# Optimization experiments

Hardware: AMD Instinct MI355X
Metric: run time of the kernel (lower is better)

The kernel has to match this reference:

```python
import jax, jax.numpy as jnp
import numpy as np

N = 50000      # nodes
DEG = 12       # in-degree per node
E = N * DEG    # 600000 edges
IN_FEATS = 256
H_FEATS = 128
NUM_LAYERS = 2
BN_EPS = 1e-5
PD_EPS = 1e-6  # torch pairwise_distance eps


def _batch_norm(x):
    # BatchNorm1d(affine=False) in training mode: per-feature batch stats, biased var
    m = x.mean(axis=0)
    v = ((x - m) ** 2).mean(axis=0)
    return (x - m) / jnp.sqrt(v + BN_EPS)


def setup_inputs() -> dict:
    key = jax.random.key(0)
    ks = jax.random.split(key, 6)
    x = jax.random.normal(ks[0], (N, IN_FEATS), dtype=jnp.float32)
    # xavier-uniform-like scales
    s_init = float(np.sqrt(6.0 / (IN_FEATS + H_FEATS)))
    s_h = float(np.sqrt(6.0 / (2 * H_FEATS)))
    W_init = jax.random.uniform(ks[1], (IN_FEATS, H_FEATS), jnp.float32, -s_init, s_init)
    W0 = jax.random.uniform(ks[2], (H_FEATS, H_FEATS), jnp.float32, -s_h, s_h)
    W1 = jax.random.uniform(ks[3], (H_FEATS, H_FEATS), jnp.float32, -s_h, s_h)
    b0 = jnp.zeros((H_FEATS,), jnp.float32)
    b1 = jnp.zeros((H_FEATS,), jnp.float32)
    src = jax.random.randint(ks[4], (E,), 0, N, dtype=jnp.int32)
    dst = jnp.repeat(jnp.arange(N, dtype=jnp.int32), DEG)  # every node has in-degree DEG
    return {"x": x, "W_init": W_init, "W0": W0, "b0": b0, "W1": W1, "b1": b1,
            "src": src, "dst": dst}


def _embed_nodes(x, W_init, Ws, bs, src, dst):
    # h = act(norm(x @ init_weight)); then GraphConv(norm='none') layers
    h = jax.nn.relu(_batch_norm(x @ W_init))
    for W, b in zip(Ws, bs):
        msg = h[src] @ W                       # [E, H]
        agg = jax.ops.segment_sum(msg, dst, num_segments=N)  # sum aggregation
        h = jax.nn.relu(_batch_norm(agg + b))
    return h


def _nonparametric_embedding(x, src, dst, deg):
    # GIN(apply_func=None, eps=-1, aggregator='mean') == mean of in-neighbors
    h = jax.nn.relu(_batch_norm(x))
    for _ in range(NUM_LAYERS):
        agg = jax.ops.segment_sum(h[src], dst, num_segments=N) / deg[:, None]
        h = jax.nn.relu(_batch_norm(agg))
    return h


def _mean_edge_dist(h, src, dst, deg):
    # apply_edges: pairwise_distance(src, dst); pull: scatter-mean onto dst
    d = jnp.linalg.norm(h[src] - h[dst] + PD_EPS, axis=1)  # [E]
    return jax.ops.segment_sum(d, dst, num_segments=N) / deg  # [N]


def reference(x, W_init, W0, b0, W1, b1, src, dst):
    deg = jnp.maximum(
        jax.ops.segment_sum(jnp.ones((E,), jnp.float32), dst, num_segments=N), 1.0)
    h_final = _embed_nodes(x, W_init, (W0, W1), (b0, b1), src, dst)
    # nonparametric target distances (detached in original)
    h_nonpar = _nonparametric_embedding(jax.lax.stop_gradient(x), src, dst, deg)
    d_nonpar = jax.lax.stop_gradient(_mean_edge_dist(h_nonpar, src, dst, deg))
    d_par = _mean_edge_dist(h_final, src, dst, deg)
    loss = jnp.mean((jnp.log(d_par) - jnp.log(d_nonpar)) ** 2)
    return (h_final, loss)
```

## Files before the change

### kernel.cpp

```cpp
#include <hip/hip_runtime.h>
#include <hip/hip_fp16.h>
#include <math.h>

#define DEG 12
#define BN_EPS 1e-5f
#define PD_EPS 1e-6f

using uint = unsigned int;

typedef _Float16 fp16x8 __attribute__((ext_vector_type(8)));
typedef float f32x2 __attribute__((ext_vector_type(2)));
typedef float f32x4 __attribute__((ext_vector_type(4)));

__device__ inline float2 h2f2(uint u) {
  __half2 h; __builtin_memcpy(&h, &u, 4);
  return __half22float2(h);
}
__device__ inline uint f2h2(float a, float b) {
  __half2 h = __floats2half2_rn(a, b);
  uint u; __builtin_memcpy(&u, &h, 4);
  return u;
}
__device__ inline f32x2 q2f_lo(uint u) { return __builtin_amdgcn_cvt_pk_f32_fp8(u, false); }
__device__ inline f32x2 q2f_hi(uint u) { return __builtin_amdgcn_cvt_pk_f32_fp8(u, true); }
__device__ inline uint f4_to_q(float a, float b, float c, float d) {
  uint w = 0;
  w = __builtin_amdgcn_cvt_pk_fp8_f32(a, b, w, false);
  w = __builtin_amdgcn_cvt_pk_fp8_f32(c, d, w, true);
  return w;
}

#define STATS_NB 256

template<int F>
__global__ __launch_bounds__(512) void stats_h_part(const __half* __restrict__ in,
                                                    float* __restrict__ parts, int M) {
  const int G = F / 8;
  __shared__ float redA[512 * 8];
  __shared__ float redB[512 * 8];
  int tid = threadIdx.x;
  int total = M * G;
  float s[8] = {0,0,0,0,0,0,0,0}, q[8] = {0,0,0,0,0,0,0,0};
  for (int i = blockIdx.x * 512 + tid; i < total; i += gridDim.x * 512) {
    uint4 raw = ((const uint4*)in)[i];
    float2 v0 = h2f2(raw.x), v1 = h2f2(raw.y), v2 = h2f2(raw.z), v3 = h2f2(raw.w);
    float v[8] = {v0.x, v0.y, v1.x, v1.y, v2.x, v2.y, v3.x, v3.y};
#pragma unroll
    for (int j = 0; j < 8; ++j) { s[j] += v[j]; q[j] += v[j] * v[j]; }
  }
#pragma unroll
  for (int j = 0; j < 8; ++j) { redA[tid * 8 + j] = s[j]; redB[tid * 8 + j] = q[j]; }
  __syncthreads();
  if (tid < F) {
    int c = tid >> 3, j = tid & 7;
    float as = 0.f, aq = 0.f;
#pragma unroll 4
    for (int r = 0; r < 512 / G; ++r) {
      as += redA[(r * G + c) * 8 + j];
      aq += redB[(r * G + c) * 8 + j];
    }
    parts[blockIdx.x * 2 * F + tid]     = as;
    parts[blockIdx.x * 2 * F + F + tid] = aq;
  }
}

template<int F>
__global__ __launch_bounds__(512) void stats_q_part(const uint* __restrict__ in,
                                                    float* __restrict__ parts, int M) {
  const int G = F / 8;
  __shared__ float redA[512 * 8];
  __shared__ float redB[512 * 8];
  int tid = threadIdx.x;
  int total = M * G;
  float s[8] = {0,0,0,0,0,0,0,0}, q[8] = {0,0,0,0,0,0,0,0};
  for (int i = blockIdx.x * 512 + tid; i < total; i += gridDim.x * 512) {
    uint2 raw = ((const uint2*)in)[i];
    f32x2 a = q2f_lo(raw.x), b = q2f_hi(raw.x), c = q2f_lo(raw.y), d = q2f_hi(raw.y);
    float v[8] = {a.x, a.y, b.x, b.y, c.x, c.y, d.x, d.y};
#pragma unroll
    for (int j = 0; j < 8; ++j) { s[j] += v[j]; q[j] += v[j] * v[j]; }
  }
#pragma unroll
  for (int j = 0; j < 8; ++j) { redA[tid * 8 + j] = s[j]; redB[tid * 8 + j] = q[j]; }
  __syncthreads();
  if (tid < F) {
    int c = tid >> 3, j = tid & 7;
    float as = 0.f, aq = 0.f;
#pragma unroll 4
    for (int r = 0; r < 512 / G; ++r) {
      as += redA[(r * G + c) * 8 + j];
      aq += redB[(r * G + c) * 8 + j];
    }
    parts[blockIdx.x * 2 * F + tid]     = as;
    parts[blockIdx.x * 2 * F + F + tid] = aq;
  }
}

template<int F>
__global__ __launch_bounds__(512) void stats_f_part(const float* __restrict__ in,
                                                    float* __restrict__ parts, int M) {
  const int G = F / 4;
  __shared__ float redA[512 * 4];
  __shared__ float redB[512 * 4];
  int tid = threadIdx.x;
  int total = M * G;
  float s[4] = {0,0,0,0}, q[4] = {0,0,0,0};
  for (int i = blockIdx.x * 512 + tid; i < total; i += gridDim.x * 512) {
    float4 v = ((const float4*)in)[i];
    float w[4] = {v.x, v.y, v.z, v.w};
#pragma unroll
    for (int j = 0; j < 4; ++j) { s[j] += w[j]; q[j] += w[j] * w[j]; }
  }
#pragma unroll
  for (int j = 0; j < 4; ++j) { redA[tid * 4 + j] = s[j]; redB[tid * 4 + j] = q[j]; }
  __syncthreads();
  if (tid < F) {
    int c = tid >> 2, j = tid & 3;
    float as = 0.f, aq = 0.f;
#pragma unroll 4
    for (int r = 0; r < 512 / G; ++r) {
      as += redA[(r * G + c) * 4 + j];
      aq += redB[(r * G + c) * 4 + j];
    }
    parts[blockIdx.x * 2 * F + tid]     = as;
    parts[blockIdx.x * 2 * F + F + tid] = aq;
  }
}

template<int F>
__global__ __launch_bounds__(1024) void stats_final(const float* __restrict__ parts,
                                                    int M, float* __restrict__ stats) {
  const int OUT = 2 * F;
  const int T   = 1024 / OUT;
  __shared__ float red[1024];
  int tid = threadIdx.x;
  int o = tid & (OUT - 1);
  int c = tid / OUT;
  float s = 0.f;
#pragma unroll 16
  for (int b = c; b < STATS_NB; b += T) s += parts[b * OUT + o];
  red[tid] = s;
  __syncthreads();
  if (tid < OUT) {
    float acc = red[tid];
#pragma unroll
    for (int cc = 1; cc < T; ++cc) acc += red[cc * OUT + tid];
    red[tid] = acc;
  }
  __syncthreads();
  if (tid < F) {
    float mean = red[tid] / (float)M;
    float var  = red[F + tid] / (float)M - mean * mean;
    stats[tid]     = mean;
    stats[F + tid] = 1.0f / sqrtf(var + BN_EPS);
  }
}

__global__ void transpose_cast(const float* __restrict__ W, __half* __restrict__ WT, int K) {
  int idx = blockIdx.x * 256 + threadIdx.x;
  if (idx >= 128 * K) return;
  int n = idx / K, k = idx - n * K;
  WT[idx] = __float2half(W[(size_t)k * 128 + n]);
}

__global__ __launch_bounds__(256) void gemm_x(
    const float* __restrict__ A, const float* __restrict__ stats,
    const __half* __restrict__ WT, __half* __restrict__ C,
    uint* __restrict__ xq, int M) {
  __shared__ uint4 Bs4[64 * 32];
  char* Bs = (char*)Bs4;
  int tid = threadIdx.x;
  int wave = tid >> 6, lane = tid & 63;
  int row0 = blockIdx.x * 64 + wave * 16;
  int r = lane & 15, kg = lane >> 4;
  int arow = row0 + r; if (arow >= M) arow = M - 1;
  bool vrow = (row0 + r) < M;
  const float* Ap = A + (size_t)arow * 256 + kg * 8;

  fp16x8 af[8];
#pragma unroll
  for (int a = 0; a < 8; ++a) {
    int c0 = kg * 8 + a * 32;
    float4 lo = *(const float4*)(Ap + a * 32);
    float4 hi = *(const float4*)(Ap + a * 32 + 4);
    af[a][0] = (_Float16)lo.x; af[a][1] = (_Float16)lo.y;
    af[a][2] = (_Float16)lo.z; af[a][3] = (_Float16)lo.w;
    af[a][4] = (_Float16)hi.x; af[a][5] = (_Float16)hi.y;
    af[a][6] = (_Float16)hi.z; af[a][7] = (_Float16)hi.w;
    float4 m0 = *(const float4*)(stats + c0);
    float4 m1 = *(const float4*)(stats + c0 + 4);
    float4 v0 = *(const float4*)(stats + 256 + c0);
    float4 v1 = *(const float4*)(stats + 256 + c0 + 4);
    float w0 = fmaxf((lo.x - m0.x) * v0.x, 0.f);
    float w1 = fmaxf((lo.y - m0.y) * v0.y, 0.f);
    float w2 = fmaxf((lo.z - m0.z) * v0.z, 0.f);
    float w3 = fmaxf((lo.w - m0.w) * v0.w, 0.f);
    float w4 = fmaxf((hi.x - m1.x) * v1.x, 0.f);
    float w5 = fmaxf((hi.y - m1.y) * v1.y, 0.f);
    float w6 = fmaxf((hi.z - m1.z) * v1.z, 0.f);
    float w7 = fmaxf((hi.w - m1.w) * v1.w, 0.f);
    if (vrow) {
      uint2 q; q.x = f4_to_q(w0, w1, w2, w3); q.y = f4_to_q(w4, w5, w6, w7);
      ((uint2*)xq)[(size_t)arow * 32 + (c0 >> 3)] = q;
    }
  }

  f32x4 acc[8];
#pragma unroll
  for (int n = 0; n < 8; ++n) acc[n] = (f32x4){0.f, 0.f, 0.f, 0.f};
  const uint4* Wg = (const uint4*)WT;

#pragma unroll
  for (int ph = 0; ph < 2; ++ph) {
    __syncthreads();
#pragma unroll
    for (int i = 0; i < 8; ++i) {
      int idx = tid + i * 256;
      int rw = idx >> 5, c16 = idx & 31;
      *(uint4*)(Bs + rw * 512 + ((c16 * 16) ^ ((rw & 7) << 4))) = Wg[ph * 2048 + idx];
    }
    __syncthreads();
#pragma unroll
    for (int a = 0; a < 8; ++a) {
#pragma unroll
      for (int n4 = 0; n4 < 4; ++n4) {
        int rw = n4 * 16 + r;
        fp16x8 bf = *(const fp16x8*)(Bs + rw * 512 + ((kg * 16 + a * 64) ^ ((r & 7) << 4)));
        acc[ph * 4 + n4] = __builtin_amdgcn_mfma_f32_16x16x32_f16(af[a], bf, acc[ph * 4 + n4], 0, 0, 0);
      }
    }
  }
#pragma unroll
  for (int n = 0; n < 8; ++n) {
    int col = n * 16 + r;
#pragma unroll
    for (int rr = 0; rr < 4; ++rr) {
      int row = row0 + kg * 4 + rr;
      if (row < M) C[(size_t)row * 128 + col] = __float2half(acc[n][rr]);
    }
  }
}

template<bool OUT_HALF>
__global__ __launch_bounds__(256) void gemm_128(
    const __half* __restrict__ A, const __half* __restrict__ WT,
    const float* __restrict__ bias, void* __restrict__ Cv, int M) {
  __shared__ uint4 Bs4[128 * 16];
  char* Bs = (char*)Bs4;
  int tid = threadIdx.x;
  const uint4* Wg = (const uint4*)WT;
#pragma unroll
  for (int i = 0; i < 8; ++i) {
    int idx = tid + i * 256;
    int rw = idx >> 4, c16 = idx & 15;
    *(uint4*)(Bs + rw * 256 + ((c16 * 16) ^ ((rw & 7) << 4))) = Wg[idx];
  }
  int wave = tid >> 6, lane = tid & 63;
  int row0 = blockIdx.x * 64 + wave * 16;
  int r = lane & 15, kg = lane >> 4;
  int arow = row0 + r; if (arow >= M) arow = M - 1;
  const _Float16* Ap = (const _Float16*)A + (size_t)arow * 128 + kg * 8;

  fp16x8 af[4];
#pragma unroll
  for (int a = 0; a < 4; ++a) af[a] = *(const fp16x8*)(Ap + a * 32);

  __syncthreads();
  f32x4 acc[8];
#pragma unroll
  for (int n = 0; n < 8; ++n) acc[n] = (f32x4){0.f, 0.f, 0.f, 0.f};
#pragma unroll
  for (int a = 0; a < 4; ++a) {
#pragma unroll
    for (int n = 0; n < 8; ++n) {
      int rw = n * 16 + r;
      fp16x8 bf = *(const fp16x8*)(Bs + rw * 256 + ((kg * 16 + a * 64) ^ ((r & 7) << 4)));
      acc[n] = __builtin_amdgcn_mfma_f32_16x16x32_f16(af[a], bf, acc[n], 0, 0, 0);
    }
  }
#pragma unroll
  for (int n = 0; n < 8; ++n) {
    int col = n * 16 + r;
    float bv = bias[col];
#pragma unroll
    for (int rr = 0; rr < 4; ++rr) {
      int row = row0 + kg * 4 + rr;
      if (row >= M) continue;
      float v = acc[n][rr] + bv;
      if (OUT_HALF) ((__half*)Cv)[(size_t)row * 128 + col] = __float2half(v);
      else          ((float*)Cv)[(size_t)row * 128 + col] = v;
    }
  }
}

template<int F, bool BNRELU>
__global__ __launch_bounds__(256) void agg_n(
    const __half* __restrict__ H, const float* __restrict__ stats,
    const int* __restrict__ src, __half* __restrict__ outh,
    float scale, int n_nodes) {
  const int LPN = F / 8;
  const int NPB = 256 / LPN;
  int tid  = threadIdx.x;
  int g    = tid / LPN;
  int lig  = tid % LPN;
  int node = blockIdx.x * NPB + g;
  if (node >= n_nodes) return;
  float m[8], iv[8];
  if (BNRELU) {
#pragma unroll
    for (int j = 0; j < 8; ++j) {
      m[j]  = stats[lig * 8 + j];
      iv[j] = stats[F + lig * 8 + j];
    }
  }
  int lane = tid & 63;
  int grpStart = lane & (63 ^ (LPN - 1));
  int se = 0;
  if ((lane & (LPN - 1)) < DEG) se = src[node * DEG + (lane & (LPN - 1))];

  const uint4* HH = (const uint4*)H;
  float a[8] = {0,0,0,0,0,0,0,0};
#pragma unroll
  for (int e = 0; e < DEG; ++e) {
    int s = __shfl(se, grpStart + e);
    uint4 raw = HH[(size_t)s * LPN + lig];
    float2 v0 = h2f2(raw.x), v1 = h2f2(raw.y), v2 = h2f2(raw.z), v3 = h2f2(raw.w);
    float w[8] = {v0.x, v0.y, v1.x, v1.y, v2.x, v2.y, v3.x, v3.y};
    if (BNRELU) {
#pragma unroll
      for (int j = 0; j < 8; ++j) w[j] = fmaxf((w[j] - m[j]) * iv[j], 0.f);
    }
#pragma unroll
    for (int j = 0; j < 8; ++j) a[j] += w[j];
  }
  uint4 w;
  w.x = f2h2(a[0] * scale, a[1] * scale);
  w.y = f2h2(a[2] * scale, a[3] * scale);
  w.z = f2h2(a[4] * scale, a[5] * scale);
  w.w = f2h2(a[6] * scale, a[7] * scale);
  ((uint4*)outh)[(size_t)node * LPN + lig] = w;
}

template<int F, bool BNRELU>
__global__ __launch_bounds__(256) void agg_q(
    const uint* __restrict__ H, const float* __restrict__ stats,
    const int* __restrict__ src, uint* __restrict__ outq,
    float scale, int n_nodes) {
  const int LPN = F / 8;
  const int NPB = 256 / LPN;
  int tid  = threadIdx.x;
  int g    = tid / LPN;
  int lig  = tid % LPN;
  int node = blockIdx.x * NPB + g;
  if (node >= n_nodes) return;
  float m[8], iv[8];
  if (BNRELU) {
#pragma unroll
    for (int j = 0; j < 8; ++j) {
      m[j]  = stats[lig * 8 + j];
      iv[j] = stats[F + lig * 8 + j];
    }
  }
  int lane = tid & 63;
  int grpStart = lane & (63 ^ (LPN - 1));
  int se = 0;
  if ((lane & (LPN - 1)) < DEG) se = src[node * DEG + (lane & (LPN - 1))];

  const uint2* HH = (const uint2*)H;
  float a[8] = {0,0,0,0,0,0,0,0};
#pragma unroll
  for (int e = 0; e < DEG; ++e) {
    int s = __shfl(se, grpStart + e);
    uint2 raw = HH[(size_t)s * LPN + lig];
    f32x2 p0 = q2f_lo(raw.x), p1 = q2f_hi(raw.x), p2 = q2f_lo(raw.y), p3 = q2f_hi(raw.y);
    float w[8] = {p0.x, p0.y, p1.x, p1.y, p2.x, p2.y, p3.x, p3.y};
    if (BNRELU) {
#pragma unroll
      for (int j = 0; j < 8; ++j) w[j] = fmaxf((w[j] - m[j]) * iv[j], 0.f);
    }
#pragma unroll
    for (int j = 0; j < 8; ++j) a[j] += w[j];
  }
  uint2 w;
  w.x = f4_to_q(a[0] * scale, a[1] * scale, a[2] * scale, a[3] * scale);
  w.y = f4_to_q(a[4] * scale, a[5] * scale, a[6] * scale, a[7] * scale);
  ((uint2*)outq)[(size_t)node * LPN + lig] = w;
}

template<int F>
__global__ __launch_bounds__(256) void dist_q(
    const uint* __restrict__ H, const int* __restrict__ src,
    float* __restrict__ out, int n_nodes) {
  const int LPN = 16;
  const int NPB = 256 / LPN;
  const int NU2 = F / 128;
  int tid  = threadIdx.x;
  int g    = tid / LPN;
  int lig  = tid % LPN;
  int node = blockIdx.x * NPB + g;
  if (node >= n_nodes) return;
  int lane = tid & 63;
  int grpStart = lane & 48;
  int se = 0;
  if ((lane & 15) < DEG) se = src[node * DEG + (lane & 15)];

  const uint2* HH = (const uint2*)H;
  float oe[NU2 * 8];
#pragma unroll
  for (int k = 0; k < NU2; ++k) {
    uint2 o = HH[(size_t)node * (F / 8) + lig * NU2 + k];
    f32x2 p0 = q2f_lo(o.x), p1 = q2f_hi(o.x), p2 = q2f_lo(o.y), p3 = q2f_hi(o.y);
    oe[k*8+0] = PD_EPS - p0.x; oe[k*8+1] = PD_EPS - p0.y;
    oe[k*8+2] = PD_EPS - p1.x; oe[k*8+3] = PD_EPS - p1.y;
    oe[k*8+4] = PD_EPS - p2.x; oe[k*8+5] = PD_EPS - p2.y;
    oe[k*8+6] = PD_EPS - p3.x; oe[k*8+7] = PD_EPS - p3.y;
  }

  float dsum = 0.f;
#pragma unroll
  for (int e = 0; e < DEG; ++e) {
    int s = __shfl(se, grpStart + e);
    float sq = 0.f;
#pragma unroll
    for (int k = 0; k < NU2; ++k) {
      uint2 raw = HH[(size_t)s * (F / 8) + lig * NU2 + k];
      f32x2 p0 = q2f_lo(raw.x), p1 = q2f_hi(raw.x), p2 = q2f_lo(raw.y), p3 = q2f_hi(raw.y);
      float w[8] = {p0.x, p0.y, p1.x, p1.y, p2.x, p2.y, p3.x, p3.y};
#pragma unroll
      for (int j = 0; j < 8; ++j) {
        float d = w[j] + oe[k*8+j];
        sq = fmaf(d, d, sq);
      }
    }
#pragma unroll
    for (int mask = 1; mask < LPN; mask <<= 1) sq += __shfl_xor(sq, mask);
    dsum += sqrtf(sq);
  }
  if (lig == 0) out[node] = dsum * (1.0f / (float)DEG);
}

template<int F>
__global__ void bnrelu_q2q(const uint* __restrict__ in, const float* __restrict__ stats,
                           uint* __restrict__ out, int total1) {
  for (int idx = blockIdx.x * blockDim.x + threadIdx.x; idx < total1;
       idx += gridDim.x * blockDim.x) {
    uint raw = in[idx];
    int f0 = (idx & (F / 4 - 1)) * 4;
    f32x2 p0 = q2f_lo(raw), p1 = q2f_hi(raw);
    float w0 = fmaxf((p0.x - stats[f0+0]) * stats[F+f0+0], 0.f);
    float w1 = fmaxf((p0.y - stats[f0+1]) * stats[F+f0+1], 0.f);
    float w2 = fmaxf((p1.x - stats[f0+2]) * stats[F+f0+2], 0.f);
    float w3 = fmaxf((p1.y - stats[f0+3]) * stats[F+f0+3], 0.f);
    out[idx] = f4_to_q(w0, w1, w2, w3);
  }
}

template<int F>
__global__ void bnrelu_dual(const float* __restrict__ in, const float* __restrict__ stats,
                            float* __restrict__ outf, uint* __restrict__ outq, int total4) {
  for (int idx = blockIdx.x * blockDim.x + threadIdx.x; idx < total4;
       idx += gridDim.x * blockDim.x) {
    float4 v = ((const float4*)in)[idx];
    int f0 = (idx & (F / 4 - 1)) * 4;
    float w0 = fmaxf((v.x - stats[f0+0]) * stats[F+f0+0], 0.f);
    float w1 = fmaxf((v.y - stats[f0+1]) * stats[F+f0+1], 0.f);
    float w2 = fmaxf((v.z - stats[f0+2]) * stats[F+f0+2], 0.f);
    float w3 = fmaxf((v.w - stats[f0+3]) * stats[F+f0+3], 0.f);
    ((float4*)outf)[idx] = make_float4(w0, w1, w2, w3);
    outq[idx] = f4_to_q(w0, w1, w2, w3);
  }
}

__global__ void loss_partial(const float* __restrict__ dpar, const float* __restrict__ dnp,
                             float* __restrict__ parts, int n) {
  __shared__ float red[256];
  float acc = 0.f;
  for (int i = blockIdx.x * 256 + threadIdx.x; i < n; i += gridDim.x * 256) {
    float t = logf(dpar[i]) - logf(dnp[i]);
    acc += t * t;
  }
  red[threadIdx.x] = acc;
  __syncthreads();
  for (int s = 128; s; s >>= 1) {
    if (threadIdx.x < s) red[threadIdx.x] += red[threadIdx.x + s];
    __syncthreads();
  }
  if (threadIdx.x == 0) parts[blockIdx.x] = red[0];
}

__global__ void loss_final(const float* __restrict__ parts, int nb,
                           float* __restrict__ out, float inv_n) {
  if (threadIdx.x == 0) {
    float s = 0.f;
    for (int i = 0; i < nb; ++i) s += parts[i];
    *out = s * inv_n;
  }
}

extern "C" void kernel_launch(void* const* d_in, const int* in_sizes, int n_in,
                              void* d_out, int out_size, void* d_ws, size_t ws_size,
                              hipStream_t stream) {
  const float* x  = (const float*)d_in[0];
  const float* Wi = (const float*)d_in[1];
  const float* W0 = (const float*)d_in[2];
  const float* b0 = (const float*)d_in[3];
  const float* W1 = (const float*)d_in[4];
  const float* b1 = (const float*)d_in[5];
  const int*  src = (const int*)d_in[6];

  const int N = in_sizes[0] / 256;
  float* out = (float*)d_out;

  const size_t NF = (size_t)N * 128;
  float* S1 = (float*)d_ws;
  float* S2 = S1 + NF;
  float* S3 = S2 + NF;
  float* aux = S3 + NF;
  float* dpar   = aux;
  float* dnp    = dpar + N;
  float* parts  = dnp + N;
  float* s_x    = parts + STATS_NB * 512;
  float* s_y0   = s_x + 512;
  float* s_z1   = s_y0 + 256;
  float* s_z2   = s_z1 + 256;
  float* s_a1   = s_z2 + 256;
  float* s_a2   = s_a1 + 512;
  float* lparts = s_a2 + 512;
  __half* WiT   = (__half*)(lparts + 64);
  __half* W0T   = (__half*)(lparts + 64 + 16384);
  __half* W1T   = (__half*)(lparts + 64 + 24576);
  uint*   xq    = (uint*)(lparts + 64 + 32768);

  __half* y0h = (__half*)S1;
  __half* H0h = (__half*)S2;
  __half* z1h = (__half*)S1;
  __half* H1h = (__half*)S2;
  float*  z2  = S3;
  uint* hq   = (uint*)S1;
  uint* A1q  = (uint*)S3;
  uint* A2q  = (uint*)S2;
  uint* A2nq = (uint*)S1;

  const int g64   = (N + 63) / 64;
  const int g128a = N / 16;
  const int gaggq = N / 8;
  const int gdist = N / 16;

  transpose_cast<<<(128 * 256 + 255) / 256, 256, 0, stream>>>(Wi, WiT, 256);
  transpose_cast<<<(128 * 128 + 255) / 256, 256, 0, stream>>>(W0, W0T, 128);
  transpose_cast<<<(128 * 128 + 255) / 256, 256, 0, stream>>>(W1, W1T, 128);

  stats_f_part<256><<<STATS_NB, 512, 0, stream>>>(x, parts, N);
  stats_final<256><<<1, 1024, 0, stream>>>(parts, N, s_x);

  gemm_x<<<g64, 256, 0, stream>>>(x, s_x, WiT, y0h, xq, N);
  stats_h_part<128><<<STATS_NB, 512, 0, stream>>>(y0h, parts, N);
  stats_final<128><<<1, 1024, 0, stream>>>(parts, N, s_y0);
  agg_n<128, true><<<g128a, 256, 0, stream>>>(y0h, s_y0, src, H0h, 1.0f, N);
  gemm_128<true><<<g64, 256, 0, stream>>>(H0h, W0T, b0, z1h, N);
  stats_h_part<128><<<STATS_NB, 512, 0, stream>>>(z1h, parts, N);
  stats_final<128><<<1, 1024, 0, stream>>>(parts, N, s_z1);
  agg_n<128, true><<<g128a, 256, 0, stream>>>(z1h, s_z1, src, H1h, 1.0f, N);
  gemm_128<false><<<g64, 256, 0, stream>>>(H1h, W1T, b1, z2, N);
  stats_f_part<128><<<STATS_NB, 512, 0, stream>>>(z2, parts, N);
  stats_final<128><<<1, 1024, 0, stream>>>(parts, N, s_z2);
  bnrelu_dual<128><<<2048, 256, 0, stream>>>(z2, s_z2, out, hq, N * 32);
  dist_q<128><<<gdist, 256, 0, stream>>>(hq, src, dpar, N);

  agg_q<256, false><<<gaggq, 256, 0, stream>>>(xq, nullptr, src, A1q, 1.0f / DEG, N);
  stats_q_part<256><<<STATS_NB, 512, 0, stream>>>(A1q, parts, N);
  stats_final<256><<<1, 1024, 0, stream>>>(parts, N, s_a1);
  agg_q<256, true><<<gaggq, 256, 0, stream>>>(A1q, s_a1, src, A2q, 1.0f / DEG, N);
  stats_q_part<256><<<STATS_NB, 512, 0, stream>>>(A2q, parts, N);
  stats_final<256><<<1, 1024, 0, stream>>>(parts, N, s_a2);
  bnrelu_q2q<256><<<2048, 256, 0, stream>>>(A2q, s_a2, A2nq, N * 64);
  dist_q<256><<<gdist, 256, 0, stream>>>(A2nq, src, dnp, N);

  loss_partial<<<64, 256, 0, stream>>>(dpar, dnp, lparts, N);
  loss_final<<<1, 64, 0, stream>>>(lparts, 64, out + (size_t)N * 128, 1.0f / (float)N);
}
```

Measured before the change: 277.2 us.

## Fuse column statistics into GEMM epilogues and store last GEMM output in half

Each GEMM now reduces per-column sums and sums of squares of its fp32 accumulators into per-block partials. A final reduction over g64 blocks replaces the separate stats pass that re-read the fp16 output. The last GEMM writes fp16 instead of fp32, and the BN/ReLU pass reads it with 8-wide loads. The three weight transposes are merged into one launch. This removes three stats kernels and part of the memory traffic, but adds shared-memory reductions and syncs to every GEMM block, gives stats_final about 780 partials to sum instead of 256, and rounds z2 to fp16 before normalization.

```diff
diff --git a/kernel.cpp b/kernel.cpp
--- a/kernel.cpp
+++ b/kernel.cpp
@@ -31,38 +31,6 @@
 }
 
 #define STATS_NB 256
-
-template<int F>
-__global__ __launch_bounds__(512) void stats_h_part(const __half* __restrict__ in,
-                                                    float* __restrict__ parts, int M) {
-  const int G = F / 8;
-  __shared__ float redA[512 * 8];
-  __shared__ float redB[512 * 8];
-  int tid = threadIdx.x;
-  int total = M * G;
-  float s[8] = {0,0,0,0,0,0,0,0}, q[8] = {0,0,0,0,0,0,0,0};
-  for (int i = blockIdx.x * 512 + tid; i < total; i += gridDim.x * 512) {
-    uint4 raw = ((const uint4*)in)[i];
-    float2 v0 = h2f2(raw.x), v1 = h2f2(raw.y), v2 = h2f2(raw.z), v3 = h2f2(raw.w);
-    float v[8] = {v0.x, v0.y, v1.x, v1.y, v2.x, v2.y, v3.x, v3.y};
-#pragma unroll
-    for (int j = 0; j < 8; ++j) { s[j] += v[j]; q[j] += v[j] * v[j]; }
-  }
-#pragma unroll
-  for (int j = 0; j < 8; ++j) { redA[tid * 8 + j] = s[j]; redB[tid * 8 + j] = q[j]; }
-  __syncthreads();
-  if (tid < F) {
-    int c = tid >> 3, j = tid & 7;
-    float as = 0.f, aq = 0.f;
-#pragma unroll 4
-    for (int r = 0; r < 512 / G; ++r) {
-      as += redA[(r * G + c) * 8 + j];
-      aq += redB[(r * G + c) * 8 + j];
-    }
-    parts[blockIdx.x * 2 * F + tid]     = as;
-    parts[blockIdx.x * 2 * F + F + tid] = aq;
-  }
-}
 
 template<int F>
 __global__ __launch_bounds__(512) void stats_q_part(const uint* __restrict__ in,
@@ -129,7 +97,7 @@
 
 template<int F>
 __global__ __launch_bounds__(1024) void stats_final(const float* __restrict__ parts,
-                                                    int M, float* __restrict__ stats) {
+                                                    int nb, int M, float* __restrict__ stats) {
   const int OUT = 2 * F;
   const int T   = 1024 / OUT;
   __shared__ float red[1024];
@@ -138,7 +106,7 @@
   int c = tid / OUT;
   float s = 0.f;
 #pragma unroll 16
-  for (int b = c; b < STATS_NB; b += T) s += parts[b * OUT + o];
+  for (int b = c; b < nb; b += T) s += parts[(size_t)b * OUT + o];
   red[tid] = s;
   __syncthreads();
   if (tid < OUT) {
@@ -156,17 +124,67 @@
   }
 }
 
-__global__ void transpose_cast(const float* __restrict__ W, __half* __restrict__ WT, int K) {
+__global__ void transpose_all(const float* __restrict__ Wi, const float* __restrict__ W0,
+                              const float* __restrict__ W1, __half* __restrict__ WiT,
+                              __half* __restrict__ W0T, __half* __restrict__ W1T) {
   int idx = blockIdx.x * 256 + threadIdx.x;
-  if (idx >= 128 * K) return;
-  int n = idx / K, k = idx - n * K;
-  WT[idx] = __float2half(W[(size_t)k * 128 + n]);
+  if (idx < 32768) {
+    int n = idx / 256, k = idx - n * 256;
+    WiT[idx] = __float2half(Wi[(size_t)k * 128 + n]);
+  } else if (idx < 49152) {
+    int i = idx - 32768; int n = i / 128, k = i - n * 128;
+    W0T[i] = __float2half(W0[(size_t)k * 128 + n]);
+  } else if (idx < 65536) {
+    int i = idx - 49152; int n = i / 128, k = i - n * 128;
+    W1T[i] = __float2half(W1[(size_t)k * 128 + n]);
+  }
+}
+
+__device__ __forceinline__ void colstats_epilogue_128(
+    void* scratch, const f32x4* acc, int row0w, int M,
+    float* __restrict__ parts, int bid, int tid, int kg, int r) {
+  float* red = (float*)scratch;
+  int slot = (tid >> 6) * 4 + kg;
+  __syncthreads();
+#pragma unroll
+  for (int n = 0; n < 8; ++n) {
+    float s = 0.f;
+#pragma unroll
+    for (int rr = 0; rr < 4; ++rr)
+      if (row0w + kg * 4 + rr < M) s += acc[n][rr];
+    red[slot * 128 + n * 16 + r] = s;
+  }
+  __syncthreads();
+  if (tid < 128) {
+    float s = 0.f;
+#pragma unroll
+    for (int i = 0; i < 16; ++i) s += red[i * 128 + tid];
+    parts[(size_t)bid * 256 + tid] = s;
+  }
+  __syncthreads();
+#pragma unroll
+  for (int n = 0; n < 8; ++n) {
+    float q = 0.f;
+#pragma unroll
+    for (int rr = 0; rr < 4; ++rr) {
+      float v = (row0w + kg * 4 + rr < M) ? acc[n][rr] : 0.f;
+      q += v * v;
+    }
+    red[slot * 128 + n * 16 + r] = q;
+  }
+  __syncthreads();
+  if (tid < 128) {
+    float q = 0.f;
+#pragma unroll
+    for (int i = 0; i < 16; ++i) q += red[i * 128 + tid];
+    parts[(size_t)bid * 256 + 128 + tid] = q;
+  }
 }
 
 __global__ __launch_bounds__(256) void gemm_x(
     const float* __restrict__ A, const float* __restrict__ stats,
     const __half* __restrict__ WT, __half* __restrict__ C,
-    uint* __restrict__ xq, int M) {
+    uint* __restrict__ xq, float* __restrict__ parts, int M) {
   __shared__ uint4 Bs4[64 * 32];
   char* Bs = (char*)Bs4;
   int tid = threadIdx.x;
@@ -239,12 +257,13 @@
       if (row < M) C[(size_t)row * 128 + col] = __float2half(acc[n][rr]);
     }
   }
-}
-
-template<bool OUT_HALF>
+  colstats_epilogue_128(Bs, acc, row0, M, parts, blockIdx.x, tid, kg, r);
+}
+
 __global__ __launch_bounds__(256) void gemm_128(
     const __half* __restrict__ A, const __half* __restrict__ WT,
-    const float* __restrict__ bias, void* __restrict__ Cv, int M) {
+    const float* __restrict__ bias, __half* __restrict__ C,
+    float* __restrict__ parts, int M) {
   __shared__ uint4 Bs4[128 * 16];
   char* Bs = (char*)Bs4;
   int tid = threadIdx.x;
@@ -284,13 +303,12 @@
     float bv = bias[col];
 #pragma unroll
     for (int rr = 0; rr < 4; ++rr) {
+      acc[n][rr] += bv;
       int row = row0 + kg * 4 + rr;
-      if (row >= M) continue;
-      float v = acc[n][rr] + bv;
-      if (OUT_HALF) ((__half*)Cv)[(size_t)row * 128 + col] = __float2half(v);
-      else          ((float*)Cv)[(size_t)row * 128 + col] = v;
-    }
-  }
+      if (row < M) C[(size_t)row * 128 + col] = __float2half(acc[n][rr]);
+    }
+  }
+  colstats_epilogue_128(Bs, acc, row0, M, parts, blockIdx.x, tid, kg, r);
 }
 
 template<int F, bool BNRELU>
@@ -456,18 +474,25 @@
 }
 
 template<int F>
-__global__ void bnrelu_dual(const float* __restrict__ in, const float* __restrict__ stats,
-                            float* __restrict__ outf, uint* __restrict__ outq, int total4) {
-  for (int idx = blockIdx.x * blockDim.x + threadIdx.x; idx < total4;
+__global__ void bnrelu_dual_h(const __half* __restrict__ in, const float* __restrict__ stats,
+                              float* __restrict__ outf, uint* __restrict__ outq, int total8) {
+  for (int idx = blockIdx.x * blockDim.x + threadIdx.x; idx < total8;
        idx += gridDim.x * blockDim.x) {
-    float4 v = ((const float4*)in)[idx];
-    int f0 = (idx & (F / 4 - 1)) * 4;
-    float w0 = fmaxf((v.x - stats[f0+0]) * stats[F+f0+0], 0.f);
-    float w1 = fmaxf((v.y - stats[f0+1]) * stats[F+f0+1], 0.f);
-    float w2 = fmaxf((v.z - stats[f0+2]) * stats[F+f0+2], 0.f);
-    float w3 = fmaxf((v.w - stats[f0+3]) * stats[F+f0+3], 0.f);
-    ((float4*)outf)[idx] = make_float4(w0, w1, w2, w3);
-    outq[idx] = f4_to_q(w0, w1, w2, w3);
+    uint4 raw = ((const uint4*)in)[idx];
+    int f0 = (idx & (F / 8 - 1)) * 8;
+    float2 v0 = h2f2(raw.x), v1 = h2f2(raw.y), v2 = h2f2(raw.z), v3 = h2f2(raw.w);
+    float w0 = fmaxf((v0.x - stats[f0+0]) * stats[F+f0+0], 0.f);
+    float w1 = fmaxf((v0.y - stats[f0+1]) * stats[F+f0+1], 0.f);
+    float w2 = fmaxf((v1.x - stats[f0+2]) * stats[F+f0+2], 0.f);
+    float w3 = fmaxf((v1.y - stats[f0+3]) * stats[F+f0+3], 0.f);
+    float w4 = fmaxf((v2.x - stats[f0+4]) * stats[F+f0+4], 0.f);
+    float w5 = fmaxf((v2.y - stats[f0+5]) * stats[F+f0+5], 0.f);
+    float w6 = fmaxf((v3.x - stats[f0+6]) * stats[F+f0+6], 0.f);
+    float w7 = fmaxf((v3.y - stats[f0+7]) * stats[F+f0+7], 0.f);
+    ((float4*)outf)[idx * 2]     = make_float4(w0, w1, w2, w3);
+    ((float4*)outf)[idx * 2 + 1] = make_float4(w4, w5, w6, w7);
+    uint2 q; q.x = f4_to_q(w0, w1, w2, w3); q.y = f4_to_q(w4, w5, w6, w7);
+    ((uint2*)outq)[idx] = q;
   }
 }
 
@@ -511,6 +536,8 @@
   const int N = in_sizes[0] / 256;
   float* out = (float*)d_out;
 
+  const int g64 = (N + 63) / 64;
+
   const size_t NF = (size_t)N * 128;
   float* S1 = (float*)d_ws;
   float* S2 = S1 + NF;
@@ -519,7 +546,7 @@
   float* dpar   = aux;
   float* dnp    = dpar + N;
   float* parts  = dnp + N;
-  float* s_x    = parts + STATS_NB * 512;
+  float* s_x    = parts + 204800;
   float* s_y0   = s_x + 512;
   float* s_z1   = s_y0 + 256;
   float* s_z2   = s_z1 + 256;
@@ -535,44 +562,38 @@
   __half* H0h = (__half*)S2;
   __half* z1h = (__half*)S1;
   __half* H1h = (__half*)S2;
-  float*  z2  = S3;
+  __half* z2h = (__half*)S3;
   uint* hq   = (uint*)S1;
   uint* A1q  = (uint*)S3;
   uint* A2q  = (uint*)S2;
   uint* A2nq = (uint*)S1;
 
-  const int g64   = (N + 63) / 64;
   const int g128a = N / 16;
   const int gaggq = N / 8;
   const int gdist = N / 16;
 
-  transpose_cast<<<(128 * 256 + 255) / 256, 256, 0, stream>>>(Wi, WiT, 256);
-  transpose_cast<<<(128 * 128 + 255) / 256, 256, 0, stream>>>(W0, W0T, 128);
-  transpose_cast<<<(128 * 128 + 255) / 256, 256, 0, stream>>>(W1, W1T, 128);
+  transpose_all<<<256, 256, 0, stream>>>(Wi, W0, W1, WiT, W0T, W1T);
 
   stats_f_part<256><<<STATS_NB, 512, 0, stream>>>(x, parts, N);
-  stats_final<256><<<1, 1024, 0, stream>>>(parts, N, s_x);
-
-  gemm_x<<<g64, 256, 0, stream>>>(x, s_x, WiT, y0h, xq, N);
-  stats_h_part<128><<<STATS_NB, 512, 0, stream>>>(y0h, parts, N);
-  stats_final<128><<<1, 1024, 0, stream>>>(parts, N, s_y0);
+  stats_final<256><<<1, 1024, 0, stream>>>(parts, STATS_NB, N, s_x);
+
+  gemm_x<<<g64, 256, 0, stream>>>(x, s_x, WiT, y0h, xq, parts, N);
+  stats_final<128><<<1, 1024, 0, stream>>>(parts, g64, N, s_y0);
   agg_n<128, true><<<g128a, 256, 0, stream>>>(y0h, s_y0, src, H0h, 1.0f, N);
-  gemm_128<true><<<g64, 256, 0, stream>>>(H0h, W0T, b0, z1h, N);
-  stats_h_part<128><<<STATS_NB, 512, 0, stream>>>(z1h, parts, N);
-  stats_final<128><<<1, 1024, 0, stream>>>(parts, N, s_z1);
+  gemm_128<<<g64, 256, 0, stream>>>(H0h, W0T, b0, z1h, parts, N);
+  stats_final<128><<<1, 1024, 0, stream>>>(parts, g64, N, s_z1);
   agg_n<128, true><<<g128a, 256, 0, stream>>>(z1h, s_z1, src, H1h, 1.0f, N);
-  gemm_128<false><<<g64, 256, 0, stream>>>(H1h, W1T, b1, z2, N);
-  stats_f_part<128><<<STATS_NB, 512, 0, stream>>>(z2, parts, N);
-  stats_final<128><<<1, 1024, 0, stream>>>(parts, N, s_z2);
-  bnrelu_dual<128><<<2048, 256, 0, stream>>>(z2, s_z2, out, hq, N * 32);
+  gemm_128<<<g64, 256, 0, stream>>>(H1h, W1T, b1, z2h, parts, N);
+  stats_final<128><<<1, 1024, 0, stream>>>(parts, g64, N, s_z2);
+  bnrelu_dual_h<128><<<2048, 256, 0, stream>>>(z2h, s_z2, out, hq, N * 16);
   dist_q<128><<<gdist, 256, 0, stream>>>(hq, src, dpar, N);
 
   agg_q<256, false><<<gaggq, 256, 0, stream>>>(xq, nullptr, src, A1q, 1.0f / DEG, N);
   stats_q_part<256><<<STATS_NB, 512, 0, stream>>>(A1q, parts, N);
-  stats_final<256><<<1, 1024, 0, stream>>>(parts, N, s_a1);
+  stats_final<256><<<1, 1024, 0, stream>>>(parts, STATS_NB, N, s_a1);
   agg_q<256, true><<<gaggq, 256, 0, stream>>>(A1q, s_a1, src, A2q, 1.0f / DEG, N);
   stats_q_part<256><<<STATS_NB, 512, 0, stream>>>(A2q, parts, N);
-  stats_final<256><<<1, 1024, 0, stream>>>(parts, N, s_a2);
+  stats_final<256><<<1, 1024, 0, stream>>>(parts, STATS_NB, N, s_a2);
   bnrelu_q2q<256><<<2048, 256, 0, stream>>>(A2q, s_a2, A2nq, N * 64);
   dist_q<256><<<gdist, 256, 0, stream>>>(A2nq, src, dnp, N);
 
```

Result: no change. 275.2 us (median of 2 runs) (-0.7%).
